# Kernel tuning notes

Measured on AMD Instinct MI355X. Metric: run time of the kernel, lower is better.

The kernel has to match this reference:

```python
import jax, jax.numpy as jnp
import numpy as np

THRESH_FACTOR = 0.7  # standard TTQ threshold: 0.7 * mean(|W|)

def ternary_quantize(w):
    delta = THRESH_FACTOR * jnp.mean(jnp.abs(w))
    # {-1, 0, +1} ternary weights
    return jnp.where(w > delta, 1.0, jnp.where(w < -delta, -1.0, 0.0)).astype(w.dtype)

def setup_inputs() -> dict:
    key = jax.random.key(0)
    k1, k2, k3 = jax.random.split(key, 3)
    B, S, D_IN, D_OUT = 8, 4096, 1024, 1024
    inp = {
        "input": jax.random.normal(k1, (B, S, D_IN), dtype=jnp.float32),
        "weight": jax.random.normal(k2, (D_OUT, D_IN), dtype=jnp.float32) * (1.0 / np.sqrt(D_IN)),
        "alpha": jnp.ones((1,), dtype=jnp.float32),
        "bias": jax.random.normal(k3, (D_OUT,), dtype=jnp.float32) * (1.0 / np.sqrt(D_IN)),
    }
    return inp

def reference(input, weight, alpha, bias):
    w_ternary = ternary_quantize(weight)          # [out, in] in {-1,0,1}
    w_eff = w_ternary * alpha                     # scalar alpha scale
    # F.linear: y = x @ W^T + b
    out = jnp.einsum('bsd,od->bso', input, w_eff) + bias
    return out
```

## Files before the change

### kernel.cpp

```cpp
#include <hip/hip_runtime.h>
#include <hip/hip_bf16.h>

typedef __bf16 bf16;
typedef __attribute__((ext_vector_type(8))) __bf16 bf16x8;
typedef __attribute__((ext_vector_type(4))) __bf16 bf16x4;
typedef __attribute__((ext_vector_type(4))) float f32x4;

#define BAR() __builtin_amdgcn_s_barrier()

__device__ __forceinline__ void async_load16(const void* g, void* l) {
    __builtin_amdgcn_global_load_lds(
        (const __attribute__((address_space(1))) void*)g,
        (__attribute__((address_space(3))) void*)l, 16, 0, 0);
}

__global__ __launch_bounds__(256) void k_absconv(const float* __restrict__ w, int wn,
                                                 double* __restrict__ part,
                                                 const float* __restrict__ x,
                                                 bf16* __restrict__ abf, int na8) {
    if (blockIdx.x < 256) {
        __shared__ double sd[256];
        const int per_block = wn / 256;
        const int base = blockIdx.x * per_block;
        double s = 0.0;
        for (int i = threadIdx.x; i < per_block; i += 256)
            s += (double)fabsf(w[base + i]);
        sd[threadIdx.x] = s;
        __syncthreads();
        for (int off = 128; off > 0; off >>= 1) {
            if (threadIdx.x < off) sd[threadIdx.x] += sd[threadIdx.x + off];
            __syncthreads();
        }
        if (threadIdx.x == 0) part[blockIdx.x] = sd[0];
    } else if (abf != nullptr) {
        const int cb     = blockIdx.x - 256;
        const int stride = (gridDim.x - 256) * 256;
        for (int i = cb * 256 + threadIdx.x; i < na8; i += stride) {
            const float4 a = ((const float4*)x)[2 * i];
            const float4 b = ((const float4*)x)[2 * i + 1];
            bf16x8 h;
            h[0] = (bf16)a.x; h[1] = (bf16)a.y; h[2] = (bf16)a.z; h[3] = (bf16)a.w;
            h[4] = (bf16)b.x; h[5] = (bf16)b.y; h[6] = (bf16)b.z; h[7] = (bf16)b.w;
            ((bf16x8*)abf)[i] = h;
        }
    }
}

__global__ __launch_bounds__(256) void k_quantW(const float* __restrict__ w,
                                                const double* __restrict__ part,
                                                bf16* __restrict__ wt, int n4, int wn) {
    __shared__ double sd[256];
    sd[threadIdx.x] = part[threadIdx.x];
    __syncthreads();
    for (int off = 128; off > 0; off >>= 1) {
        if (threadIdx.x < off) sd[threadIdx.x] += sd[threadIdx.x + off];
        __syncthreads();
    }
    const float d = (float)(0.7 * sd[0] / (double)wn);
    const int stride = gridDim.x * 256;
    for (int i = blockIdx.x * 256 + threadIdx.x; i < n4; i += stride) {
        const float4 v = ((const float4*)w)[i];
        bf16x4 o;
        o[0] = (bf16)((v.x > d) ? 1.0f : (v.x < -d) ? -1.0f : 0.0f);
        o[1] = (bf16)((v.y > d) ? 1.0f : (v.y < -d) ? -1.0f : 0.0f);
        o[2] = (bf16)((v.z > d) ? 1.0f : (v.z < -d) ? -1.0f : 0.0f);
        o[3] = (bf16)((v.w > d) ? 1.0f : (v.w < -d) ? -1.0f : 0.0f);
        *(bf16x4*)(wt + (size_t)i * 4) = o;
    }
}

__device__ __forceinline__ void stage_half(const bf16* __restrict__ srch, int K, int kt,
                                           char* dst, int t) {
    #pragma unroll
    for (int r = 0; r < 2; ++r) {
        const int c  = (r << 9) + t;
        const int rp = c >> 3;
        const int s  = (c & 7) ^ ((t >> 3) & 7);
        async_load16(srch + (size_t)rp * K + (kt << 6) + (s << 3), dst + (c << 4));
    }
}

__global__ __launch_bounds__(512, 4) void k_gemm2(const bf16* __restrict__ A,
                                                  const bf16* __restrict__ Bw,
                                                  const float* __restrict__ alphap,
                                                  const float* __restrict__ bias,
                                                  float* __restrict__ C,
                                                  int M, int N, int K) {
    __shared__ __align__(16) char As[16384];
    __shared__ __align__(16) char Bs[32768];

    const int t    = threadIdx.x;
    const int lane = t & 63;
    const int w    = t >> 6;
    const int wm   = w >> 2;
    const int wn   = w & 3;
    const int lr   = lane & 15;
    const int hi   = lane >> 4;

    const int nbn = N >> 8;
    const int cpx = gridDim.x >> 3;
    const int lid = (blockIdx.x & 7) * cpx + (blockIdx.x >> 3);
    const int bn0 = (lid % nbn) << 8;
    const int bm0 = (lid / nbn) << 7;

    const bf16* Asrc  = A  + (size_t)bm0 * K;
    const bf16* Bsrc0 = Bw + (size_t)bn0 * K;
    const bf16* Bsrc1 = Bw + (size_t)(bn0 + 128) * K;

    f32x4 acc[4][4] = {};
    bf16x8 af[4], bf[4];

    const int x0 = ((hi ^ (lr & 7)) << 4);
    const int x1 = (((4 + hi) ^ (lr & 7)) << 4);

#define RDA(XS) do { \
    _Pragma("unroll") \
    for (int m = 0; m < 4; ++m) { \
        const int _r = (wm << 6) + (m << 4) + lr; \
        af[m] = *(const bf16x8*)(As + _r * 128 + (XS)); \
    } \
} while (0)

#define RDB(XS) do { \
    _Pragma("unroll") \
    for (int n = 0; n < 4; ++n) { \
        const int _r = (wn << 6) + (n << 4) + lr; \
        bf[n] = *(const bf16x8*)(Bs + _r * 128 + (XS)); \
    } \
} while (0)

#define MF16() do { \
    __builtin_amdgcn_s_setprio(1); \
    _Pragma("unroll") \
    for (int m = 0; m < 4; ++m) \
        _Pragma("unroll") \
        for (int n = 0; n < 4; ++n) \
            acc[m][n] = __builtin_amdgcn_mfma_f32_16x16x32_bf16(af[m], bf[n], acc[m][n], 0, 0, 0); \
    __builtin_amdgcn_s_setprio(0); \
} while (0)

#define VMCNT0() asm volatile("s_waitcnt vmcnt(0)" ::: "memory")
#define LGKM0()  asm volatile("s_waitcnt lgkmcnt(0)" ::: "memory")

    stage_half(Asrc,  K, 0, As, t);
    stage_half(Bsrc0, K, 0, Bs, t);
    stage_half(Bsrc1, K, 0, Bs + 16384, t);
    VMCNT0();
    BAR();

    const int NT = K >> 6;
    for (int kt = 0; kt < NT; ++kt) {
        const bool more = (kt + 1) < NT;

        RDA(x0); RDB(x0);
        MF16();
        RDA(x1); RDB(x1);
        LGKM0();
        BAR();
        if (more) {
            stage_half(Asrc,  K, kt + 1, As, t);
            stage_half(Bsrc0, K, kt + 1, Bs, t);
            stage_half(Bsrc1, K, kt + 1, Bs + 16384, t);
        }
        MF16();
        if (more) { VMCNT0(); }
        BAR();
    }

    const float alpha = *alphap;
    float bv[4];
    #pragma unroll
    for (int nf = 0; nf < 4; ++nf) bv[nf] = bias[bn0 + (wn << 6) + (nf << 4) + lr];

    #pragma unroll
    for (int mf = 0; mf < 4; ++mf) {
        const int grow = bm0 + (wm << 6) + (mf << 4) + (hi << 2);
        #pragma unroll
        for (int nf = 0; nf < 4; ++nf) {
            const int gcol = bn0 + (wn << 6) + (nf << 4) + lr;
            #pragma unroll
            for (int r = 0; r < 4; ++r)
                C[(size_t)(grow + r) * N + gcol] = alpha * acc[mf][nf][r] + bv[nf];
        }
    }
#undef RDA
#undef RDB
#undef MF16
#undef VMCNT0
#undef LGKM0
}

__global__ __launch_bounds__(256) void k_gemm_fb(const float* __restrict__ A,
                                                 const bf16* __restrict__ Bw,
                                                 const float* __restrict__ alphap,
                                                 const float* __restrict__ bias,
                                                 float* __restrict__ C,
                                                 int M, int N, int K) {
    __shared__ bf16 As[128 * 32];
    __shared__ bf16 Bs[128 * 32];
    const int t = threadIdx.x, lane = t & 63, wave = t >> 6;
    const int nbm = M >> 7;
    const int bm0 = (blockIdx.x % nbm) << 7;
    const int bn0 = (blockIdx.x / nbm) << 7;
    const int wr = (wave >> 1) << 6, wc = (wave & 1) << 6;
    f32x4 acc[4][4] = {};
    const int lr = lane & 15, lk = (lane >> 4) << 3;
    for (int k0 = 0; k0 < K; k0 += 32) {
        #pragma unroll
        for (int j = 0; j < 2; ++j) {
            const int c = t + j * 256;
            async_load16(Bw + (size_t)(bn0 + (c >> 2)) * K + k0 + ((c & 3) << 3),
                         (char*)Bs + j * 4096 + wave * 1024);
        }
        #pragma unroll
        for (int i = 0; i < 4; ++i) {
            const int idx = t + i * 256;
            const int row = idx >> 3, c4 = (idx & 7) << 2;
            const float4 v = *(const float4*)(A + (size_t)(bm0 + row) * K + k0 + c4);
            bf16x4 h;
            h[0] = (bf16)v.x; h[1] = (bf16)v.y; h[2] = (bf16)v.z; h[3] = (bf16)v.w;
            *(bf16x4*)(As + row * 32 + c4) = h;
        }
        __syncthreads();
        bf16x8 af[4], bfr[4];
        #pragma unroll
        for (int m = 0; m < 4; ++m) af[m] = *(const bf16x8*)(As + (wr + m * 16 + lr) * 32 + lk);
        #pragma unroll
        for (int n = 0; n < 4; ++n) bfr[n] = *(const bf16x8*)(Bs + (wc + n * 16 + lr) * 32 + lk);
        #pragma unroll
        for (int m = 0; m < 4; ++m)
            #pragma unroll
            for (int n = 0; n < 4; ++n)
                acc[m][n] = __builtin_amdgcn_mfma_f32_16x16x32_bf16(af[m], bfr[n], acc[m][n], 0, 0, 0);
        __syncthreads();
    }
    const float alpha = *alphap;
    #pragma unroll
    for (int m = 0; m < 4; ++m)
        #pragma unroll
        for (int n = 0; n < 4; ++n) {
            const int gcol = bn0 + wc + n * 16 + lr;
            const float bv = bias[gcol];
            #pragma unroll
            for (int r = 0; r < 4; ++r) {
                const int grow = bm0 + wr + m * 16 + ((lane >> 4) << 2) + r;
                C[(size_t)grow * N + gcol] = alpha * acc[m][n][r] + bv;
            }
        }
}

extern "C" void kernel_launch(void* const* d_in, const int* in_sizes, int n_in,
                              void* d_out, int out_size, void* d_ws, size_t ws_size,
                              hipStream_t stream) {
    const float* x     = (const float*)d_in[0];
    const float* wgt   = (const float*)d_in[1];
    const float* alpha = (const float*)d_in[2];
    const float* bias  = (const float*)d_in[3];
    float* out = (float*)d_out;

    const int wn   = in_sizes[1];
    const int dout = in_sizes[3];
    const int din  = wn / dout;
    const int m    = in_sizes[0] / din;

    char* ws = (char*)d_ws;
    double* part = (double*)(ws + 64);
    bf16*   wt   = (bf16*)(ws + 8192);
    bf16*   abf  = (bf16*)(ws + (4u << 20));

    const size_t need = (4u << 20) + (size_t)in_sizes[0] * 2;
    const bool use2 = (ws_size >= need) && (m % 128) == 0 && (dout % 256) == 0 &&
                      (din % 64) == 0 && ((m / 128) * (dout / 256)) % 8 == 0;

    if (use2) {
        k_absconv<<<2304, 256, 0, stream>>>(wgt, wn, part, x, abf, in_sizes[0] / 8);
        k_quantW<<<512, 256, 0, stream>>>(wgt, part, wt, wn / 4, wn);
        dim3 grid((m / 128) * (dout / 256));
        k_gemm2<<<grid, 512, 0, stream>>>(abf, wt, alpha, bias, out, m, dout, din);
    } else {
        k_absconv<<<256, 256, 0, stream>>>(wgt, wn, part, x, nullptr, 0);
        k_quantW<<<512, 256, 0, stream>>>(wgt, part, wt, wn / 4, wn);
        dim3 grid((m / 128) * (dout / 128));
        k_gemm_fb<<<grid, 256, 0, stream>>>(x, wt, alpha, bias, out, m, dout, din);
    }
}
```

Measured before the change: 115.7 us.

## Fuse fp32-to-bf16 activation conversion into GEMM A-tile staging

Drops the separate pass that converted the whole fp32 activation to a bf16 workspace buffer. The GEMM now loads fp32 A rows through registers, converts them to bf16 and writes them into swizzled LDS. Loads for the next k-tile are issued before the current tile's MFMAs so their latency is partly hidden. The block tile shrinks to 64x256 with 256 threads and B is staged asynchronously with more loads per thread. This removes a 128MB read plus 64MB write round trip, but A traffic per tile doubles in bytes, and the smaller M tile means B is reread more often.

```diff
diff --git a/kernel.cpp b/kernel.cpp
--- a/kernel.cpp
+++ b/kernel.cpp
@@ -14,36 +14,21 @@
         (__attribute__((address_space(3))) void*)l, 16, 0, 0);
 }
 
-__global__ __launch_bounds__(256) void k_absconv(const float* __restrict__ w, int wn,
-                                                 double* __restrict__ part,
-                                                 const float* __restrict__ x,
-                                                 bf16* __restrict__ abf, int na8) {
-    if (blockIdx.x < 256) {
-        __shared__ double sd[256];
-        const int per_block = wn / 256;
-        const int base = blockIdx.x * per_block;
-        double s = 0.0;
-        for (int i = threadIdx.x; i < per_block; i += 256)
-            s += (double)fabsf(w[base + i]);
-        sd[threadIdx.x] = s;
-        __syncthreads();
-        for (int off = 128; off > 0; off >>= 1) {
-            if (threadIdx.x < off) sd[threadIdx.x] += sd[threadIdx.x + off];
-            __syncthreads();
-        }
-        if (threadIdx.x == 0) part[blockIdx.x] = sd[0];
-    } else if (abf != nullptr) {
-        const int cb     = blockIdx.x - 256;
-        const int stride = (gridDim.x - 256) * 256;
-        for (int i = cb * 256 + threadIdx.x; i < na8; i += stride) {
-            const float4 a = ((const float4*)x)[2 * i];
-            const float4 b = ((const float4*)x)[2 * i + 1];
-            bf16x8 h;
-            h[0] = (bf16)a.x; h[1] = (bf16)a.y; h[2] = (bf16)a.z; h[3] = (bf16)a.w;
-            h[4] = (bf16)b.x; h[5] = (bf16)b.y; h[6] = (bf16)b.z; h[7] = (bf16)b.w;
-            ((bf16x8*)abf)[i] = h;
-        }
-    }
+__global__ __launch_bounds__(256) void k_abs_part(const float* __restrict__ w, int n,
+                                                  double* __restrict__ part) {
+    __shared__ double sd[256];
+    const int per_block = n / gridDim.x;
+    const int base = blockIdx.x * per_block;
+    double s = 0.0;
+    for (int i = threadIdx.x; i < per_block; i += 256)
+        s += (double)fabsf(w[base + i]);
+    sd[threadIdx.x] = s;
+    __syncthreads();
+    for (int off = 128; off > 0; off >>= 1) {
+        if (threadIdx.x < off) sd[threadIdx.x] += sd[threadIdx.x + off];
+        __syncthreads();
+    }
+    if (threadIdx.x == 0) part[blockIdx.x] = sd[0];
 }
 
 __global__ __launch_bounds__(256) void k_quantW(const float* __restrict__ w,
@@ -69,31 +54,29 @@
     }
 }
 
-__device__ __forceinline__ void stage_half(const bf16* __restrict__ srch, int K, int kt,
+__device__ __forceinline__ void stage_B128(const bf16* __restrict__ srch, int K, int kt,
                                            char* dst, int t) {
     #pragma unroll
-    for (int r = 0; r < 2; ++r) {
-        const int c  = (r << 9) + t;
+    for (int r = 0; r < 4; ++r) {
+        const int c  = (r << 8) + t;
         const int rp = c >> 3;
         const int s  = (c & 7) ^ ((t >> 3) & 7);
         async_load16(srch + (size_t)rp * K + (kt << 6) + (s << 3), dst + (c << 4));
     }
 }
 
-__global__ __launch_bounds__(512, 4) void k_gemm2(const bf16* __restrict__ A,
+__global__ __launch_bounds__(256, 4) void k_gemmF(const float* __restrict__ Afp,
                                                   const bf16* __restrict__ Bw,
                                                   const float* __restrict__ alphap,
                                                   const float* __restrict__ bias,
                                                   float* __restrict__ C,
                                                   int M, int N, int K) {
-    __shared__ __align__(16) char As[16384];
+    __shared__ __align__(16) char As[8192];
     __shared__ __align__(16) char Bs[32768];
 
     const int t    = threadIdx.x;
     const int lane = t & 63;
-    const int w    = t >> 6;
-    const int wm   = w >> 2;
-    const int wn   = w & 3;
+    const int wn   = t >> 6;
     const int lr   = lane & 15;
     const int hi   = lane >> 4;
 
@@ -101,32 +84,42 @@
     const int cpx = gridDim.x >> 3;
     const int lid = (blockIdx.x & 7) * cpx + (blockIdx.x >> 3);
     const int bn0 = (lid % nbn) << 8;
-    const int bm0 = (lid / nbn) << 7;
-
-    const bf16* Asrc  = A  + (size_t)bm0 * K;
-    const bf16* Bsrc0 = Bw + (size_t)bn0 * K;
-    const bf16* Bsrc1 = Bw + (size_t)(bn0 + 128) * K;
+    const int bm0 = (lid / nbn) << 6;
+
+    const int a_r = t >> 2;
+    const int a_q = t & 3;
+    const float* Asrc  = Afp + (size_t)(bm0 + a_r) * K + (a_q << 4);
+    const bf16*  Bsrc0 = Bw + (size_t)bn0 * K;
+    const bf16*  Bsrc1 = Bw + (size_t)(bn0 + 128) * K;
 
     f32x4 acc[4][4] = {};
     bf16x8 af[4], bf[4];
+    float4 s0, s1;
 
     const int x0 = ((hi ^ (lr & 7)) << 4);
     const int x1 = (((4 + hi) ^ (lr & 7)) << 4);
+    char* a_d0 = As + a_r * 128 + ((((a_q << 1))     ^ (a_r & 7)) << 4);
+    char* a_d1 = As + a_r * 128 + ((((a_q << 1) | 1) ^ (a_r & 7)) << 4);
+
+#define LA_H0(KT) do { const float* _p = Asrc + ((KT) << 6); \
+    s0 = *(const float4*)_p; s1 = *(const float4*)(_p + 4); } while (0)
+#define LA_H1(KT) do { const float* _p = Asrc + ((KT) << 6) + 8; \
+    s0 = *(const float4*)_p; s1 = *(const float4*)(_p + 4); } while (0)
+#define WA(D) do { bf16x8 _h; \
+    _h[0]=(bf16)s0.x; _h[1]=(bf16)s0.y; _h[2]=(bf16)s0.z; _h[3]=(bf16)s0.w; \
+    _h[4]=(bf16)s1.x; _h[5]=(bf16)s1.y; _h[6]=(bf16)s1.z; _h[7]=(bf16)s1.w; \
+    *(bf16x8*)(D) = _h; } while (0)
 
 #define RDA(XS) do { \
     _Pragma("unroll") \
-    for (int m = 0; m < 4; ++m) { \
-        const int _r = (wm << 6) + (m << 4) + lr; \
-        af[m] = *(const bf16x8*)(As + _r * 128 + (XS)); \
-    } \
+    for (int m = 0; m < 4; ++m) \
+        af[m] = *(const bf16x8*)(As + ((m << 4) + lr) * 128 + (XS)); \
 } while (0)
 
 #define RDB(XS) do { \
     _Pragma("unroll") \
-    for (int n = 0; n < 4; ++n) { \
-        const int _r = (wn << 6) + (n << 4) + lr; \
-        bf[n] = *(const bf16x8*)(Bs + _r * 128 + (XS)); \
-    } \
+    for (int n = 0; n < 4; ++n) \
+        bf[n] = *(const bf16x8*)(Bs + (((wn << 6) + (n << 4) + lr)) * 128 + (XS)); \
 } while (0)
 
 #define MF16() do { \
@@ -142,47 +135,52 @@
 #define VMCNT0() asm volatile("s_waitcnt vmcnt(0)" ::: "memory")
 #define LGKM0()  asm volatile("s_waitcnt lgkmcnt(0)" ::: "memory")
 
-    stage_half(Asrc,  K, 0, As, t);
-    stage_half(Bsrc0, K, 0, Bs, t);
-    stage_half(Bsrc1, K, 0, Bs + 16384, t);
-    VMCNT0();
+    LA_H0(0);
+    WA(a_d0);
+    LA_H1(0);
+    stage_B128(Bsrc0, K, 0, Bs, t);
+    stage_B128(Bsrc1, K, 0, Bs + 16384, t);
+    WA(a_d1);
+    VMCNT0(); LGKM0();
     BAR();
 
     const int NT = K >> 6;
     for (int kt = 0; kt < NT; ++kt) {
         const bool more = (kt + 1) < NT;
-
+        if (more) LA_H0(kt + 1);
         RDA(x0); RDB(x0);
         MF16();
         RDA(x1); RDB(x1);
         LGKM0();
         BAR();
         if (more) {
-            stage_half(Asrc,  K, kt + 1, As, t);
-            stage_half(Bsrc0, K, kt + 1, Bs, t);
-            stage_half(Bsrc1, K, kt + 1, Bs + 16384, t);
+            WA(a_d0);
+            LA_H1(kt + 1);
+            stage_B128(Bsrc0, K, kt + 1, Bs, t);
+            stage_B128(Bsrc1, K, kt + 1, Bs + 16384, t);
         }
         MF16();
-        if (more) { VMCNT0(); }
+        if (more) WA(a_d1);
+        VMCNT0(); LGKM0();
         BAR();
     }
 
     const float alpha = *alphap;
-    float bv[4];
-    #pragma unroll
-    for (int nf = 0; nf < 4; ++nf) bv[nf] = bias[bn0 + (wn << 6) + (nf << 4) + lr];
-
     #pragma unroll
     for (int mf = 0; mf < 4; ++mf) {
-        const int grow = bm0 + (wm << 6) + (mf << 4) + (hi << 2);
+        const int grow = bm0 + (mf << 4) + (hi << 2);
         #pragma unroll
         for (int nf = 0; nf < 4; ++nf) {
             const int gcol = bn0 + (wn << 6) + (nf << 4) + lr;
+            const float bv = bias[gcol];
             #pragma unroll
             for (int r = 0; r < 4; ++r)
-                C[(size_t)(grow + r) * N + gcol] = alpha * acc[mf][nf][r] + bv[nf];
-        }
-    }
+                C[(size_t)(grow + r) * N + gcol] = alpha * acc[mf][nf][r] + bv;
+        }
+    }
+#undef LA_H0
+#undef LA_H1
+#undef WA
 #undef RDA
 #undef RDB
 #undef MF16
@@ -266,20 +264,16 @@
     char* ws = (char*)d_ws;
     double* part = (double*)(ws + 64);
     bf16*   wt   = (bf16*)(ws + 8192);
-    bf16*   abf  = (bf16*)(ws + (4u << 20));
-
-    const size_t need = (4u << 20) + (size_t)in_sizes[0] * 2;
-    const bool use2 = (ws_size >= need) && (m % 128) == 0 && (dout % 256) == 0 &&
-                      (din % 64) == 0 && ((m / 128) * (dout / 256)) % 8 == 0;
-
-    if (use2) {
-        k_absconv<<<2304, 256, 0, stream>>>(wgt, wn, part, x, abf, in_sizes[0] / 8);
-        k_quantW<<<512, 256, 0, stream>>>(wgt, part, wt, wn / 4, wn);
-        dim3 grid((m / 128) * (dout / 256));
-        k_gemm2<<<grid, 512, 0, stream>>>(abf, wt, alpha, bias, out, m, dout, din);
+
+    k_abs_part<<<256, 256, 0, stream>>>(wgt, wn, part);
+    k_quantW<<<512, 256, 0, stream>>>(wgt, part, wt, wn / 4, wn);
+
+    const bool useF = (m % 64) == 0 && (dout % 256) == 0 && (din % 64) == 0 &&
+                      ((m / 64) * (dout / 256)) % 8 == 0;
+    if (useF) {
+        dim3 grid((m / 64) * (dout / 256));
+        k_gemmF<<<grid, 256, 0, stream>>>(x, wt, alpha, bias, out, m, dout, din);
     } else {
-        k_absconv<<<256, 256, 0, stream>>>(wgt, wn, part, x, nullptr, 0);
-        k_quantW<<<512, 256, 0, stream>>>(wgt, part, wt, wn / 4, wn);
         dim3 grid((m / 128) * (dout / 128));
         k_gemm_fb<<<grid, 256, 0, stream>>>(x, wt, alpha, bias, out, m, dout, din);
     }
```

Measured after the change: 215.7 us. 86.4% more time.

## Fuse fp32-to-bf16 activation conversion into GEMM A-tile staging

Applied to the files above, without the earlier changes.

Removes the separate pass that converted the fp32 activations into a bf16 workspace buffer. The GEMM now async-loads fp32 A tiles straight into LDS (a 32 KB A buffer instead of 16 KB) and converts them to bf16 while reading fragments. This drops one full write and re-read of the converted activations, which are never reused across calls. In exchange it doubles A-side global and LDS traffic inside the GEMM, adds conversion ALU work in the inner loop, and the larger LDS footprint may lower occupancy.

```diff
diff --git a/kernel.cpp b/kernel.cpp
--- a/kernel.cpp
+++ b/kernel.cpp
@@ -14,36 +14,21 @@
         (__attribute__((address_space(3))) void*)l, 16, 0, 0);
 }
 
-__global__ __launch_bounds__(256) void k_absconv(const float* __restrict__ w, int wn,
-                                                 double* __restrict__ part,
-                                                 const float* __restrict__ x,
-                                                 bf16* __restrict__ abf, int na8) {
-    if (blockIdx.x < 256) {
-        __shared__ double sd[256];
-        const int per_block = wn / 256;
-        const int base = blockIdx.x * per_block;
-        double s = 0.0;
-        for (int i = threadIdx.x; i < per_block; i += 256)
-            s += (double)fabsf(w[base + i]);
-        sd[threadIdx.x] = s;
-        __syncthreads();
-        for (int off = 128; off > 0; off >>= 1) {
-            if (threadIdx.x < off) sd[threadIdx.x] += sd[threadIdx.x + off];
-            __syncthreads();
-        }
-        if (threadIdx.x == 0) part[blockIdx.x] = sd[0];
-    } else if (abf != nullptr) {
-        const int cb     = blockIdx.x - 256;
-        const int stride = (gridDim.x - 256) * 256;
-        for (int i = cb * 256 + threadIdx.x; i < na8; i += stride) {
-            const float4 a = ((const float4*)x)[2 * i];
-            const float4 b = ((const float4*)x)[2 * i + 1];
-            bf16x8 h;
-            h[0] = (bf16)a.x; h[1] = (bf16)a.y; h[2] = (bf16)a.z; h[3] = (bf16)a.w;
-            h[4] = (bf16)b.x; h[5] = (bf16)b.y; h[6] = (bf16)b.z; h[7] = (bf16)b.w;
-            ((bf16x8*)abf)[i] = h;
-        }
-    }
+__global__ __launch_bounds__(256) void k_abs_part(const float* __restrict__ w, int n,
+                                                  double* __restrict__ part) {
+    __shared__ double sd[256];
+    const int per_block = n / gridDim.x;
+    const int base = blockIdx.x * per_block;
+    double s = 0.0;
+    for (int i = threadIdx.x; i < per_block; i += 256)
+        s += (double)fabsf(w[base + i]);
+    sd[threadIdx.x] = s;
+    __syncthreads();
+    for (int off = 128; off > 0; off >>= 1) {
+        if (threadIdx.x < off) sd[threadIdx.x] += sd[threadIdx.x + off];
+        __syncthreads();
+    }
+    if (threadIdx.x == 0) part[blockIdx.x] = sd[0];
 }
 
 __global__ __launch_bounds__(256) void k_quantW(const float* __restrict__ w,
@@ -80,13 +65,24 @@
     }
 }
 
-__global__ __launch_bounds__(512, 4) void k_gemm2(const bf16* __restrict__ A,
+__device__ __forceinline__ void stage_Afp(const float* __restrict__ srch, int K, int kt,
+                                          char* dst, int t) {
+    #pragma unroll
+    for (int r = 0; r < 4; ++r) {
+        const int c  = (r << 9) + t;
+        const int rp = c >> 4;
+        const int s  = (c & 15) ^ (((t >> 4) & 7) << 1);
+        async_load16(srch + (size_t)rp * K + (kt << 6) + (s << 2), dst + (c << 4));
+    }
+}
+
+__global__ __launch_bounds__(512, 4) void k_gemmH(const float* __restrict__ Afp,
                                                   const bf16* __restrict__ Bw,
                                                   const float* __restrict__ alphap,
                                                   const float* __restrict__ bias,
                                                   float* __restrict__ C,
                                                   int M, int N, int K) {
-    __shared__ __align__(16) char As[16384];
+    __shared__ __align__(16) char As[32768];
     __shared__ __align__(16) char Bs[32768];
 
     const int t    = threadIdx.x;
@@ -103,21 +99,29 @@
     const int bn0 = (lid % nbn) << 8;
     const int bm0 = (lid / nbn) << 7;
 
-    const bf16* Asrc  = A  + (size_t)bm0 * K;
-    const bf16* Bsrc0 = Bw + (size_t)bn0 * K;
-    const bf16* Bsrc1 = Bw + (size_t)(bn0 + 128) * K;
+    const float* Asrc  = Afp + (size_t)bm0 * K;
+    const bf16*  Bsrc0 = Bw + (size_t)bn0 * K;
+    const bf16*  Bsrc1 = Bw + (size_t)(bn0 + 128) * K;
 
     f32x4 acc[4][4] = {};
     bf16x8 af[4], bf[4];
 
-    const int x0 = ((hi ^ (lr & 7)) << 4);
-    const int x1 = (((4 + hi) ^ (lr & 7)) << 4);
-
-#define RDA(XS) do { \
+    const int x0  = ((hi ^ (lr & 7)) << 4);
+    const int x1  = (((4 + hi) ^ (lr & 7)) << 4);
+    const int ax0 = x0 << 1;
+    const int ax1 = x1 << 1;
+
+#define RDA_F(AXS) do { \
     _Pragma("unroll") \
     for (int m = 0; m < 4; ++m) { \
         const int _r = (wm << 6) + (m << 4) + lr; \
-        af[m] = *(const bf16x8*)(As + _r * 128 + (XS)); \
+        const char* _p = As + _r * 256 + (AXS); \
+        const f32x4 _u0 = *(const f32x4*)_p; \
+        const f32x4 _u1 = *(const f32x4*)(_p + 16); \
+        bf16x8 _h; \
+        _h[0]=(bf16)_u0[0]; _h[1]=(bf16)_u0[1]; _h[2]=(bf16)_u0[2]; _h[3]=(bf16)_u0[3]; \
+        _h[4]=(bf16)_u1[0]; _h[5]=(bf16)_u1[1]; _h[6]=(bf16)_u1[2]; _h[7]=(bf16)_u1[3]; \
+        af[m] = _h; \
     } \
 } while (0)
 
@@ -142,7 +146,7 @@
 #define VMCNT0() asm volatile("s_waitcnt vmcnt(0)" ::: "memory")
 #define LGKM0()  asm volatile("s_waitcnt lgkmcnt(0)" ::: "memory")
 
-    stage_half(Asrc,  K, 0, As, t);
+    stage_Afp(Asrc, K, 0, As, t);
     stage_half(Bsrc0, K, 0, Bs, t);
     stage_half(Bsrc1, K, 0, Bs + 16384, t);
     VMCNT0();
@@ -152,13 +156,13 @@
     for (int kt = 0; kt < NT; ++kt) {
         const bool more = (kt + 1) < NT;
 
-        RDA(x0); RDB(x0);
+        RDA_F(ax0); RDB(x0);
         MF16();
-        RDA(x1); RDB(x1);
+        RDA_F(ax1); RDB(x1);
         LGKM0();
         BAR();
         if (more) {
-            stage_half(Asrc,  K, kt + 1, As, t);
+            stage_Afp(Asrc, K, kt + 1, As, t);
             stage_half(Bsrc0, K, kt + 1, Bs, t);
             stage_half(Bsrc1, K, kt + 1, Bs + 16384, t);
         }
@@ -183,7 +187,7 @@
                 C[(size_t)(grow + r) * N + gcol] = alpha * acc[mf][nf][r] + bv[nf];
         }
     }
-#undef RDA
+#undef RDA_F
 #undef RDB
 #undef MF16
 #undef VMCNT0
@@ -266,20 +270,16 @@
     char* ws = (char*)d_ws;
     double* part = (double*)(ws + 64);
     bf16*   wt   = (bf16*)(ws + 8192);
-    bf16*   abf  = (bf16*)(ws + (4u << 20));
-
-    const size_t need = (4u << 20) + (size_t)in_sizes[0] * 2;
-    const bool use2 = (ws_size >= need) && (m % 128) == 0 && (dout % 256) == 0 &&
-                      (din % 64) == 0 && ((m / 128) * (dout / 256)) % 8 == 0;
-
-    if (use2) {
-        k_absconv<<<2304, 256, 0, stream>>>(wgt, wn, part, x, abf, in_sizes[0] / 8);
-        k_quantW<<<512, 256, 0, stream>>>(wgt, part, wt, wn / 4, wn);
+
+    k_abs_part<<<256, 256, 0, stream>>>(wgt, wn, part);
+    k_quantW<<<512, 256, 0, stream>>>(wgt, part, wt, wn / 4, wn);
+
+    const bool useH = (m % 128) == 0 && (dout % 256) == 0 && (din % 64) == 0 &&
+                      ((m / 128) * (dout / 256)) % 8 == 0;
+    if (useH) {
         dim3 grid((m / 128) * (dout / 256));
-        k_gemm2<<<grid, 512, 0, stream>>>(abf, wt, alpha, bias, out, m, dout, din);
+        k_gemmH<<<grid, 512, 0, stream>>>(x, wt, alpha, bias, out, m, dout, din);
     } else {
-        k_absconv<<<256, 256, 0, stream>>>(wgt, wn, part, x, nullptr, 0);
-        k_quantW<<<512, 256, 0, stream>>>(wgt, part, wt, wn / 4, wn);
         dim3 grid((m / 128) * (dout / 128));
         k_gemm_fb<<<grid, 256, 0, stream>>>(x, wt, alpha, bias, out, m, dout, din);
     }
```

Result: slower. 339.7 us (+193.6%).
